# Optimization experiments

Hardware: AMD Instinct MI355X
Metric: run time of the kernel (lower is better)

Reference implementation:

```python
import jax, jax.numpy as jnp
import numpy as np

N = 100000
E = 3200000
IN_DIM = 128
HD = 64
HEADS = 4
NEG_SLOPE = 0.2


def setup_inputs() -> dict:
    key = jax.random.key(0)
    ks = jax.random.split(key, 12)
    s = lambda fan_in: 1.0 / np.sqrt(fan_in)
    x = jax.random.normal(ks[0], (N, IN_DIM), dtype=jnp.float32)
    edge_index = jax.random.randint(ks[1], (2, E), 0, N, dtype=jnp.int64)
    W1 = jax.random.normal(ks[2], (IN_DIM, HEADS * HD), dtype=jnp.float32) * s(IN_DIM)
    a_src1 = jax.random.normal(ks[3], (HEADS, HD), dtype=jnp.float32) * s(HD)
    a_dst1 = jax.random.normal(ks[4], (HEADS, HD), dtype=jnp.float32) * s(HD)
    b1 = jnp.zeros((HEADS * HD,), dtype=jnp.float32)
    W2 = jax.random.normal(ks[5], (HEADS * HD, HD), dtype=jnp.float32) * s(HEADS * HD)
    a_src2 = jax.random.normal(ks[6], (1, HD), dtype=jnp.float32) * s(HD)
    a_dst2 = jax.random.normal(ks[7], (1, HD), dtype=jnp.float32) * s(HD)
    b2 = jnp.zeros((HD,), dtype=jnp.float32)
    lin_w = jax.random.normal(ks[8], (HD, 2), dtype=jnp.float32) * s(HD)
    lin_b = jnp.zeros((2,), dtype=jnp.float32)
    return {"x": x, "edge_index": edge_index, "W1": W1, "a_src1": a_src1,
            "a_dst1": a_dst1, "b1": b1, "W2": W2, "a_src2": a_src2,
            "a_dst2": a_dst2, "b2": b2, "lin_w": lin_w, "lin_b": lin_b}


def gat_conv(x, src, dst, W, a_src, a_dst, bias, heads, out_dim, concat):
    n = x.shape[0]
    h = (x @ W).reshape(n, heads, out_dim)                 # [N,H,D]
    alpha_s = jnp.einsum('nhd,hd->nh', h, a_src)           # [N,H]
    alpha_d = jnp.einsum('nhd,hd->nh', h, a_dst)           # [N,H]
    e = alpha_s[src] + alpha_d[dst]                        # [Etot,H]
    e = jnp.where(e > 0, e, NEG_SLOPE * e)                 # leaky relu
    m = jax.ops.segment_max(e, dst, num_segments=n)        # scatter-softmax (stable)
    m = jnp.where(jnp.isfinite(m), m, 0.0)
    e = jnp.exp(e - m[dst])
    denom = jax.ops.segment_sum(e, dst, num_segments=n)
    alpha = e / denom[dst]                                 # [Etot,H]
    out = jax.ops.segment_sum(h[src] * alpha[:, :, None], dst, num_segments=n)  # [N,H,D]
    out = out.reshape(n, heads * out_dim) if concat else out.mean(axis=1)
    return out + bias


def reference(x, edge_index, W1, a_src1, a_dst1, b1, W2, a_src2, a_dst2, b2, lin_w, lin_b):
    n = x.shape[0]
    loops = jnp.arange(n, dtype=edge_index.dtype)
    src = jnp.concatenate([edge_index[0], loops])          # add self-loops (PyG default)
    dst = jnp.concatenate([edge_index[1], loops])
    h = gat_conv(x, src, dst, W1, a_src1, a_dst1, b1, HEADS, HD, True)
    h = jax.nn.elu(h)
    h = gat_conv(h, src, dst, W2, a_src2, a_dst2, b2, 1, HD, True)
    h = jax.nn.elu(h)
    return h @ lin_w + lin_b                               # [N,2]
```

## Files before the change

### kernel.cpp

```cpp
#include <hip/hip_runtime.h>
#include <hip/hip_fp16.h>
#include <math.h>

#define NN 100000
#define EE 3200000
#define ETOT (EE + NN)
#define NEG_SLOPE 0.2f
#define DMAX 96
#define CHUNK 4096
#define NB0 ((ETOT + CHUNK - 1) / CHUNK)
#define RB 391
#define CAP 16384

typedef _Float16 half8 __attribute__((ext_vector_type(8)));
typedef _Float16 half4v __attribute__((ext_vector_type(4)));
typedef float floatx4 __attribute__((ext_vector_type(4)));

__device__ __forceinline__ float wsum64(float v) {
#pragma unroll
  for (int o = 32; o; o >>= 1) v += __shfl_xor(v, o);
  return v;
}
__device__ __forceinline__ float lrelu(float v) { return v > 0.f ? v : NEG_SLOPE * v; }
__device__ __forceinline__ float elu1(float v) { return v > 0.f ? v : expm1f(v); }

__global__ void k_init(int* __restrict__ ccur) {
  ccur[threadIdx.x] = threadIdx.x * CAP;
}

__global__ __launch_bounds__(256) void k_pass1(const int* __restrict__ ei,
                                               int* __restrict__ ccur,
                                               unsigned* __restrict__ ebuf,
                                               const float* __restrict__ W1,
                                               const float* __restrict__ W2,
                                               _Float16* __restrict__ W1t,
                                               _Float16* __restrict__ W2t) {
  int b = blockIdx.x;
  if (b >= NB0) {
    int idx = (b - NB0) * 256 + threadIdx.x;
    if (idx < 32768) {
      int n = idx >> 7, k = idx & 127;
      W1t[idx] = (_Float16)W1[k * 256 + n];
    } else {
      int j = idx - 32768;
      int n = j >> 8, k = j & 255;
      W2t[j] = (_Float16)W2[k * 64 + n];
    }
    return;
  }
  __shared__ int h[256];
  __shared__ int cur[256];
  int t = threadIdx.x;
  h[t] = 0;
  __syncthreads();
  int base = b * CHUNK;
  int lim = base + CHUNK; if (lim > ETOT) lim = ETOT;
  for (int e = base + t; e < lim; e += 256) {
    int d = (e < EE) ? ei[EE + e] : (e - EE);
    atomicAdd(&h[(unsigned)d / (unsigned)RB], 1);
  }
  __syncthreads();
  if (h[t]) cur[t] = atomicAdd(&ccur[t], h[t]);
  __syncthreads();
  for (int e = base + t; e < lim; e += 256) {
    int s, d;
    if (e < EE) { s = ei[e]; d = ei[EE + e]; } else { s = e - EE; d = s; }
    unsigned cb = (unsigned)d / (unsigned)RB;
    unsigned dloc = (unsigned)d - cb * (unsigned)RB;
    int pos = atomicAdd(&cur[cb], 1);
    ebuf[pos] = (dloc << 17) | (unsigned)s;
  }
}

__global__ __launch_bounds__(256) void k_pass2(const unsigned* __restrict__ ebuf,
                                               const int* __restrict__ ccur,
                                               int* __restrict__ offs,
                                               int* __restrict__ degarr,
                                               int* __restrict__ csr) {
  __shared__ unsigned ed[CAP];
  __shared__ int hist[RB];
  __shared__ int cur[RB];
  int b = blockIdx.x, t = threadIdx.x;
  int d0 = b * RB;
  int rb = NN - d0; if (rb > RB) rb = RB;
  int w0 = b * CAP;
  int cnt = ccur[b] - w0;
  if (cnt > CAP) cnt = CAP;
  for (int j = t; j < rb; j += 256) hist[j] = 0;
  __syncthreads();
  for (int i = t; i < cnt; i += 256) {
    unsigned v = ebuf[w0 + i];
    ed[i] = v;
    atomicAdd(&hist[v >> 17], 1);
  }
  __syncthreads();
  if (t == 0) {
    int run = w0;
    for (int j = 0; j < rb; ++j) { cur[j] = run; run += hist[j]; }
  }
  __syncthreads();
  for (int j = t; j < rb; j += 256) {
    offs[d0 + j] = cur[j];
    degarr[d0 + j] = hist[j];
  }
  __syncthreads();
  for (int i = t; i < cnt; i += 256) {
    unsigned v = ed[i];
    int pos = atomicAdd(&cur[v >> 17], 1);
    csr[pos] = (int)(v & 0x1FFFFu);
  }
}

__global__ __launch_bounds__(256) void k_gemm1m(const float* __restrict__ x,
                                                const _Float16* __restrict__ W1t,
                                                const float* __restrict__ a_src,
                                                const float* __restrict__ a_dst,
                                                _Float16* __restrict__ h1h,
                                                float* __restrict__ as_out,
                                                float* __restrict__ ad_out) {
  __shared__ _Float16 As[64][136];
  __shared__ _Float16 Wt[128][136];
  const int bx = blockIdx.x & 1;
  const int by = blockIdx.x >> 1;
  const int tid = threadIdx.x;
  const int row0 = by * 64;
#pragma unroll
  for (int i = 0; i < 8; ++i) {
    int idx = i * 256 + tid;
    int r = idx >> 5;
    int c4 = (idx & 31) * 4;
    int gr = row0 + r;
    float4 f = make_float4(0.f, 0.f, 0.f, 0.f);
    if (gr < NN) f = *(const float4*)(x + (size_t)gr * 128 + c4);
    half4v h; h[0] = (_Float16)f.x; h[1] = (_Float16)f.y; h[2] = (_Float16)f.z; h[3] = (_Float16)f.w;
    *(half4v*)&As[r][c4] = h;
  }
#pragma unroll
  for (int i = 0; i < 8; ++i) {
    int idx = i * 256 + tid;
    int r = idx >> 4;
    int g = idx & 15;
    *(half8*)&Wt[r][g * 8] = *(const half8*)(W1t + (size_t)(bx * 128 + r) * 128 + g * 8);
  }
  __syncthreads();

  const int wid = tid >> 6, lane = tid & 63;
  const int m16 = lane & 15, quad = lane >> 4;
  floatx4 acc[8];
#pragma unroll
  for (int nt = 0; nt < 8; ++nt) acc[nt] = (floatx4){0.f, 0.f, 0.f, 0.f};
#pragma unroll
  for (int ks = 0; ks < 4; ++ks) {
    half8 av = *(half8*)&As[wid * 16 + m16][ks * 32 + quad * 8];
#pragma unroll
    for (int nt = 0; nt < 8; ++nt) {
      half8 bv = *(half8*)&Wt[nt * 16 + m16][ks * 32 + quad * 8];
      acc[nt] = __builtin_amdgcn_mfma_f32_16x16x32_f16(av, bv, acc[nt], 0, 0, 0);
    }
  }
  float asr[8], adr[8];
#pragma unroll
  for (int nt = 0; nt < 8; ++nt) {
    asr[nt] = a_src[bx * 128 + nt * 16 + m16];
    adr[nt] = a_dst[bx * 128 + nt * 16 + m16];
  }
#pragma unroll
  for (int r = 0; r < 4; ++r) {
    int gr = row0 + wid * 16 + quad * 4 + r;
    bool ok = gr < NN;
#pragma unroll
    for (int hp = 0; hp < 2; ++hp) {
      float ps = 0.f, pd = 0.f;
#pragma unroll
      for (int j = 0; j < 4; ++j) {
        ps = fmaf(acc[hp * 4 + j][r], asr[hp * 4 + j], ps);
        pd = fmaf(acc[hp * 4 + j][r], adr[hp * 4 + j], pd);
      }
#pragma unroll
      for (int o = 1; o < 16; o <<= 1) { ps += __shfl_xor(ps, o); pd += __shfl_xor(pd, o); }
      if (ok && m16 == 0) {
        as_out[gr * 4 + bx * 2 + hp] = ps;
        ad_out[gr * 4 + bx * 2 + hp] = pd;
      }
    }
    if (ok) {
#pragma unroll
      for (int nt = 0; nt < 8; ++nt)
        h1h[(size_t)gr * 256 + bx * 128 + nt * 16 + m16] = (_Float16)acc[nt][r];
    }
  }
}

__global__ __launch_bounds__(256) void k_gemm2m(const _Float16* __restrict__ h1e,
                                                const _Float16* __restrict__ W2t,
                                                const float* __restrict__ a_src,
                                                const float* __restrict__ a_dst,
                                                _Float16* __restrict__ h2h,
                                                float* __restrict__ as_out,
                                                float* __restrict__ ad_out) {
  __shared__ _Float16 As2[64][136];
  __shared__ _Float16 Wt2[64][264];
  const int by = blockIdx.x;
  const int tid = threadIdx.x;
  const int row0 = by * 64;
#pragma unroll
  for (int i = 0; i < 8; ++i) {
    int idx = i * 256 + tid;
    int r = idx >> 5;
    int g = idx & 31;
    *(half8*)&Wt2[r][g * 8] = *(const half8*)(W2t + (size_t)r * 256 + g * 8);
  }
  const int wid = tid >> 6, lane = tid & 63;
  const int m16 = lane & 15, quad = lane >> 4;
  floatx4 acc[4];
#pragma unroll
  for (int nt = 0; nt < 4; ++nt) acc[nt] = (floatx4){0.f, 0.f, 0.f, 0.f};

  for (int kc = 0; kc < 2; ++kc) {
#pragma unroll
    for (int i = 0; i < 4; ++i) {
      int idx = i * 256 + tid;
      int r = idx >> 4;
      int g = idx & 15;
      int gr = row0 + r;
      half8 v = {0, 0, 0, 0, 0, 0, 0, 0};
      if (gr < NN) v = *(const half8*)(h1e + (size_t)gr * 256 + kc * 128 + g * 8);
      *(half8*)&As2[r][g * 8] = v;
    }
    __syncthreads();
#pragma unroll
    for (int ks = 0; ks < 4; ++ks) {
      half8 av = *(half8*)&As2[wid * 16 + m16][ks * 32 + quad * 8];
#pragma unroll
      for (int nt = 0; nt < 4; ++nt) {
        half8 bv = *(half8*)&Wt2[nt * 16 + m16][kc * 128 + ks * 32 + quad * 8];
        acc[nt] = __builtin_amdgcn_mfma_f32_16x16x32_f16(av, bv, acc[nt], 0, 0, 0);
      }
    }
    __syncthreads();
  }
  float asr[4], adr[4];
#pragma unroll
  for (int nt = 0; nt < 4; ++nt) {
    asr[nt] = a_src[nt * 16 + m16];
    adr[nt] = a_dst[nt * 16 + m16];
  }
#pragma unroll
  for (int r = 0; r < 4; ++r) {
    float ps = 0.f, pd = 0.f;
#pragma unroll
    for (int nt = 0; nt < 4; ++nt) {
      ps = fmaf(acc[nt][r], asr[nt], ps);
      pd = fmaf(acc[nt][r], adr[nt], pd);
    }
#pragma unroll
    for (int o = 1; o < 16; o <<= 1) { ps += __shfl_xor(ps, o); pd += __shfl_xor(pd, o); }
    int gr = row0 + wid * 16 + quad * 4 + r;
    if (gr < NN) {
      if (m16 == 0) { as_out[gr] = ps; ad_out[gr] = pd; }
#pragma unroll
      for (int nt = 0; nt < 4; ++nt)
        h2h[(size_t)gr * 64 + nt * 16 + m16] = (_Float16)acc[nt][r];
    }
  }
}

__global__ __launch_bounds__(256) void k_attn1(const int* __restrict__ offs,
                                               const int* __restrict__ degarr,
                                               const int* __restrict__ csr_src,
                                               const float* __restrict__ a_s,
                                               const float* __restrict__ a_d,
                                               const _Float16* __restrict__ h1h,
                                               const float* __restrict__ b1,
                                               _Float16* __restrict__ h1e) {
  __shared__ float alpha[4][DMAX][4];
  __shared__ int sidx[4][DMAX];
  const int wid = threadIdx.x >> 6;
  const int n = blockIdx.x * 4 + wid;
  const int lane = threadIdx.x & 63;
  const int beg = offs[n], deg = degarr[n];
  const float4 ad = *(const float4*)(a_d + n * 4);
  float4 sm = make_float4(0.f, 0.f, 0.f, 0.f);
  for (int d = lane; d < deg; d += 64) {
    int s = csr_src[beg + d];
    float4 as = *(const float4*)(a_s + s * 4);
    float e0 = __expf(lrelu(as.x + ad.x));
    float e1 = __expf(lrelu(as.y + ad.y));
    float e2 = __expf(lrelu(as.z + ad.z));
    float e3 = __expf(lrelu(as.w + ad.w));
    sm.x += e0; sm.y += e1; sm.z += e2; sm.w += e3;
    if (d < DMAX) {
      sidx[wid][d] = s;
      *(float4*)&alpha[wid][d][0] = make_float4(e0, e1, e2, e3);
    }
  }
  sm.x = wsum64(sm.x); sm.y = wsum64(sm.y); sm.z = wsum64(sm.z); sm.w = wsum64(sm.w);
  const float4 inv4 = make_float4(1.f / sm.x, 1.f / sm.y, 1.f / sm.z, 1.f / sm.w);
  const int dlim = deg < DMAX ? deg : DMAX;
  for (int d = lane; d < dlim; d += 64) {
    float4 a = *(float4*)&alpha[wid][d][0];
    a.x *= inv4.x; a.y *= inv4.y; a.z *= inv4.z; a.w *= inv4.w;
    *(float4*)&alpha[wid][d][0] = a;
  }
  const int h = lane >> 4;
  float4 acc = make_float4(0.f, 0.f, 0.f, 0.f);
  int d = 0;
  for (; d + 8 <= dlim; d += 8) {
    int ss[8]; float ww[8];
#pragma unroll
    for (int u = 0; u < 8; ++u) {
      ss[u] = sidx[wid][d + u];
      ww[u] = alpha[wid][d + u][h];
    }
    half4v rr[8];
#pragma unroll
    for (int u = 0; u < 8; ++u)
      rr[u] = *(const half4v*)(h1h + (size_t)ss[u] * 256 + lane * 4);
#pragma unroll
    for (int u = 0; u < 8; ++u) {
      acc.x = fmaf((float)rr[u][0], ww[u], acc.x);
      acc.y = fmaf((float)rr[u][1], ww[u], acc.y);
      acc.z = fmaf((float)rr[u][2], ww[u], acc.z);
      acc.w = fmaf((float)rr[u][3], ww[u], acc.w);
    }
  }
  for (; d < dlim; ++d) {
    int s = sidx[wid][d];
    float w = alpha[wid][d][h];
    half4v r = *(const half4v*)(h1h + (size_t)s * 256 + lane * 4);
    acc.x = fmaf((float)r[0], w, acc.x); acc.y = fmaf((float)r[1], w, acc.y);
    acc.z = fmaf((float)r[2], w, acc.z); acc.w = fmaf((float)r[3], w, acc.w);
  }
  const float adh = (h & 2) ? ((h & 1) ? ad.w : ad.z) : ((h & 1) ? ad.y : ad.x);
  const float invh = (h & 2) ? ((h & 1) ? inv4.w : inv4.z) : ((h & 1) ? inv4.y : inv4.x);
  for (; d < deg; ++d) {
    int s = csr_src[beg + d];
    float w = __expf(lrelu(a_s[s * 4 + h] + adh)) * invh;
    half4v r = *(const half4v*)(h1h + (size_t)s * 256 + lane * 4);
    acc.x = fmaf((float)r[0], w, acc.x); acc.y = fmaf((float)r[1], w, acc.y);
    acc.z = fmaf((float)r[2], w, acc.z); acc.w = fmaf((float)r[3], w, acc.w);
  }
  const int c = lane * 4;
  float4 bb = *(const float4*)(b1 + c);
  half4v o;
  o[0] = (_Float16)elu1(acc.x + bb.x);
  o[1] = (_Float16)elu1(acc.y + bb.y);
  o[2] = (_Float16)elu1(acc.z + bb.z);
  o[3] = (_Float16)elu1(acc.w + bb.w);
  *(half4v*)(h1e + (size_t)n * 256 + c) = o;
}

__global__ __launch_bounds__(256) void k_attn2(const int* __restrict__ offs,
                                               const int* __restrict__ degarr,
                                               const int* __restrict__ csr_src,
                                               const float* __restrict__ a_s,
                                               const float* __restrict__ a_d,
                                               const _Float16* __restrict__ h2h,
                                               const float* __restrict__ b2,
                                               const float* __restrict__ lin_w,
                                               const float* __restrict__ lin_b,
                                               float* __restrict__ out) {
  __shared__ float alpha2[4][DMAX];
  __shared__ int sidx2[4][DMAX];
  const int wid = threadIdx.x >> 6;
  const int n = blockIdx.x * 4 + wid;
  const int lane = threadIdx.x & 63;
  const int beg = offs[n], deg = degarr[n];
  const float adn = a_d[n];
  float sm = 0.f;
  for (int d = lane; d < deg; d += 64) {
    int s = csr_src[beg + d];
    float e = __expf(lrelu(a_s[s] + adn));
    sm += e;
    if (d < DMAX) { sidx2[wid][d] = s; alpha2[wid][d] = e; }
  }
  sm = wsum64(sm);
  const float inv = 1.f / sm;
  const int dlim = deg < DMAX ? deg : DMAX;
  for (int d = lane; d < dlim; d += 64) alpha2[wid][d] *= inv;
  const int quarter = lane >> 4;
  const int fl = lane & 15;
  float acc4[4];
#pragma unroll
  for (int i = 0; i < 4; ++i) acc4[i] = 0.f;
  for (int d = 0; d < dlim; d += 8) {
    int ss[2]; float ww[2];
#pragma unroll
    for (int u = 0; u < 2; ++u) {
      int e = d + 4 * u + quarter;
      bool valid = e < dlim;
      int e2 = valid ? e : 0;
      ss[u] = sidx2[wid][e2];
      ww[u] = valid ? alpha2[wid][e2] : 0.f;
    }
    half4v rr[2];
#pragma unroll
    for (int u = 0; u < 2; ++u)
      rr[u] = *(const half4v*)(h2h + (size_t)ss[u] * 64 + fl * 4);
#pragma unroll
    for (int u = 0; u < 2; ++u)
#pragma unroll
      for (int i = 0; i < 4; ++i)
        acc4[i] = fmaf((float)rr[u][i], ww[u], acc4[i]);
  }
  for (int d = dlim + quarter; d < deg; d += 4) {
    int s = csr_src[beg + d];
    float w = __expf(lrelu(a_s[s] + adn)) * inv;
    half4v r = *(const half4v*)(h2h + (size_t)s * 64 + fl * 4);
#pragma unroll
    for (int i = 0; i < 4; ++i) acc4[i] = fmaf((float)r[i], w, acc4[i]);
  }
#pragma unroll
  for (int i = 0; i < 4; ++i) {
    acc4[i] += __shfl_xor(acc4[i], 16);
    acc4[i] += __shfl_xor(acc4[i], 32);
  }
  float p0 = 0.f, p1 = 0.f;
#pragma unroll
  for (int i = 0; i < 4; ++i) {
    float o = elu1(acc4[i] + b2[fl * 4 + i]);
    p0 = fmaf(o, lin_w[(fl * 4 + i) * 2 + 0], p0);
    p1 = fmaf(o, lin_w[(fl * 4 + i) * 2 + 1], p1);
  }
#pragma unroll
  for (int o = 1; o < 16; o <<= 1) { p0 += __shfl_xor(p0, o); p1 += __shfl_xor(p1, o); }
  if (lane == 0) {
    out[n * 2 + 0] = p0 + lin_b[0];
    out[n * 2 + 1] = p1 + lin_b[1];
  }
}

extern "C" void kernel_launch(void* const* d_in, const int* in_sizes, int n_in,
                              void* d_out, int out_size, void* d_ws, size_t ws_size,
                              hipStream_t stream) {
  const float* x      = (const float*)d_in[0];
  const int*   ei     = (const int*)d_in[1];
  const float* W1     = (const float*)d_in[2];
  const float* a_src1 = (const float*)d_in[3];
  const float* a_dst1 = (const float*)d_in[4];
  const float* b1     = (const float*)d_in[5];
  const float* W2     = (const float*)d_in[6];
  const float* a_src2 = (const float*)d_in[7];
  const float* a_dst2 = (const float*)d_in[8];
  const float* b2     = (const float*)d_in[9];
  const float* lin_w  = (const float*)d_in[10];
  const float* lin_b  = (const float*)d_in[11];
  float* outp = (float*)d_out;

  char* w = (char*)d_ws;
  _Float16* h1h = (_Float16*)(w + 0);
  _Float16* h1e = (_Float16*)(w + 51200000);
  _Float16* h2h = (_Float16*)(w + 102400000);
  _Float16* W1t = (_Float16*)(w + 115200000);
  _Float16* W2t = (_Float16*)(w + 115265536);
  float*  as1 = (float*)(w + 115298304);
  float*  ad1 = (float*)(w + 116898304);
  float*  as2 = (float*)(w + 118498304);
  float*  ad2 = (float*)(w + 118898304);
  int*    offs = (int*)(w + 119298304);
  int*    degarr = (int*)(w + 119698304);
  int*    ccur = (int*)(w + 120098304);
  unsigned* ebuf = (unsigned*)(w + 120099328);
  int*    csr = (int*)(w + 136876544);

  k_init<<<1, 256, 0, stream>>>(ccur);
  k_pass1<<<NB0 + 192, 256, 0, stream>>>(ei, ccur, ebuf, W1, W2, W1t, W2t);
  k_pass2<<<256, 256, 0, stream>>>(ebuf, ccur, offs, degarr, csr);

  k_gemm1m<<<2 * 1563, 256, 0, stream>>>(x, W1t, a_src1, a_dst1, h1h, as1, ad1);
  k_attn1<<<NN / 4, 256, 0, stream>>>(offs, degarr, csr, as1, ad1, h1h, b1, h1e);

  k_gemm2m<<<1563, 256, 0, stream>>>(h1e, W2t, a_src2, a_dst2, h2h, as2, ad2);
  k_attn2<<<NN / 4, 256, 0, stream>>>(offs, degarr, csr, as2, ad2, h2h, b2, lin_w, lin_b, outp);
}
```

Baseline: 615.5 us.

## Use sub-wavefront groups per node in attention kernels and memset counters

```diff
diff --git a/kernel.cpp b/kernel.cpp
--- a/kernel.cpp
+++ b/kernel.cpp
@@ -16,17 +16,8 @@
 typedef _Float16 half4v __attribute__((ext_vector_type(4)));
 typedef float floatx4 __attribute__((ext_vector_type(4)));
 
-__device__ __forceinline__ float wsum64(float v) {
-#pragma unroll
-  for (int o = 32; o; o >>= 1) v += __shfl_xor(v, o);
-  return v;
-}
 __device__ __forceinline__ float lrelu(float v) { return v > 0.f ? v : NEG_SLOPE * v; }
 __device__ __forceinline__ float elu1(float v) { return v > 0.f ? v : expm1f(v); }
-
-__global__ void k_init(int* __restrict__ ccur) {
-  ccur[threadIdx.x] = threadIdx.x * CAP;
-}
 
 __global__ __launch_bounds__(256) void k_pass1(const int* __restrict__ ei,
                                                int* __restrict__ ccur,
@@ -60,7 +51,7 @@
     atomicAdd(&h[(unsigned)d / (unsigned)RB], 1);
   }
   __syncthreads();
-  if (h[t]) cur[t] = atomicAdd(&ccur[t], h[t]);
+  if (h[t]) cur[t] = t * CAP + atomicAdd(&ccur[t], h[t]);
   __syncthreads();
   for (int e = base + t; e < lim; e += 256) {
     int s, d;
@@ -84,7 +75,7 @@
   int d0 = b * RB;
   int rb = NN - d0; if (rb > RB) rb = RB;
   int w0 = b * CAP;
-  int cnt = ccur[b] - w0;
+  int cnt = ccur[b];
   if (cnt > CAP) cnt = CAP;
   for (int j = t; j < rb; j += 256) hist[j] = 0;
   __syncthreads();
@@ -273,81 +264,90 @@
                                                const _Float16* __restrict__ h1h,
                                                const float* __restrict__ b1,
                                                _Float16* __restrict__ h1e) {
-  __shared__ float alpha[4][DMAX][4];
-  __shared__ int sidx[4][DMAX];
-  const int wid = threadIdx.x >> 6;
-  const int n = blockIdx.x * 4 + wid;
-  const int lane = threadIdx.x & 63;
+  __shared__ float alpha[8][DMAX][4];
+  __shared__ int sidx[8][DMAX];
+  const int g = threadIdx.x >> 5;
+  const int gl = threadIdx.x & 31;
+  const int n = blockIdx.x * 8 + g;
   const int beg = offs[n], deg = degarr[n];
-  const float4 ad = *(const float4*)(a_d + n * 4);
+  const float4 ad = *(const float4*)(a_d + (size_t)n * 4);
   float4 sm = make_float4(0.f, 0.f, 0.f, 0.f);
-  for (int d = lane; d < deg; d += 64) {
+  for (int d = gl; d < deg; d += 32) {
     int s = csr_src[beg + d];
-    float4 as = *(const float4*)(a_s + s * 4);
+    float4 as = *(const float4*)(a_s + (size_t)s * 4);
     float e0 = __expf(lrelu(as.x + ad.x));
     float e1 = __expf(lrelu(as.y + ad.y));
     float e2 = __expf(lrelu(as.z + ad.z));
     float e3 = __expf(lrelu(as.w + ad.w));
     sm.x += e0; sm.y += e1; sm.z += e2; sm.w += e3;
     if (d < DMAX) {
-      sidx[wid][d] = s;
-      *(float4*)&alpha[wid][d][0] = make_float4(e0, e1, e2, e3);
-    }
-  }
-  sm.x = wsum64(sm.x); sm.y = wsum64(sm.y); sm.z = wsum64(sm.z); sm.w = wsum64(sm.w);
+      sidx[g][d] = s;
+      *(float4*)&alpha[g][d][0] = make_float4(e0, e1, e2, e3);
+    }
+  }
+#pragma unroll
+  for (int o = 16; o; o >>= 1) {
+    sm.x += __shfl_xor(sm.x, o); sm.y += __shfl_xor(sm.y, o);
+    sm.z += __shfl_xor(sm.z, o); sm.w += __shfl_xor(sm.w, o);
+  }
   const float4 inv4 = make_float4(1.f / sm.x, 1.f / sm.y, 1.f / sm.z, 1.f / sm.w);
   const int dlim = deg < DMAX ? deg : DMAX;
-  for (int d = lane; d < dlim; d += 64) {
-    float4 a = *(float4*)&alpha[wid][d][0];
+  for (int d = gl; d < dlim; d += 32) {
+    float4 a = *(float4*)&alpha[g][d][0];
     a.x *= inv4.x; a.y *= inv4.y; a.z *= inv4.z; a.w *= inv4.w;
-    *(float4*)&alpha[wid][d][0] = a;
-  }
-  const int h = lane >> 4;
-  float4 acc = make_float4(0.f, 0.f, 0.f, 0.f);
+    *(float4*)&alpha[g][d][0] = a;
+  }
+  const int h = gl >> 3;
+  float acc8[8];
+#pragma unroll
+  for (int i = 0; i < 8; ++i) acc8[i] = 0.f;
   int d = 0;
   for (; d + 8 <= dlim; d += 8) {
     int ss[8]; float ww[8];
 #pragma unroll
     for (int u = 0; u < 8; ++u) {
-      ss[u] = sidx[wid][d + u];
-      ww[u] = alpha[wid][d + u][h];
-    }
-    half4v rr[8];
+      ss[u] = sidx[g][d + u];
+      ww[u] = alpha[g][d + u][h];
+    }
+    half8 rr[8];
 #pragma unroll
     for (int u = 0; u < 8; ++u)
-      rr[u] = *(const half4v*)(h1h + (size_t)ss[u] * 256 + lane * 4);
-#pragma unroll
-    for (int u = 0; u < 8; ++u) {
-      acc.x = fmaf((float)rr[u][0], ww[u], acc.x);
-      acc.y = fmaf((float)rr[u][1], ww[u], acc.y);
-      acc.z = fmaf((float)rr[u][2], ww[u], acc.z);
-      acc.w = fmaf((float)rr[u][3], ww[u], acc.w);
-    }
+      rr[u] = *(const half8*)(h1h + (size_t)ss[u] * 256 + gl * 8);
+#pragma unroll
+    for (int u = 0; u < 8; ++u)
+#pragma unroll
+      for (int i = 0; i < 8; ++i)
+        acc8[i] = fmaf((float)rr[u][i], ww[u], acc8[i]);
   }
   for (; d < dlim; ++d) {
-    int s = sidx[wid][d];
-    float w = alpha[wid][d][h];
-    half4v r = *(const half4v*)(h1h + (size_t)s * 256 + lane * 4);
-    acc.x = fmaf((float)r[0], w, acc.x); acc.y = fmaf((float)r[1], w, acc.y);
-    acc.z = fmaf((float)r[2], w, acc.z); acc.w = fmaf((float)r[3], w, acc.w);
+    int s = sidx[g][d];
+    float w = alpha[g][d][h];
+    half8 r = *(const half8*)(h1h + (size_t)s * 256 + gl * 8);
+#pragma unroll
+    for (int i = 0; i < 8; ++i) acc8[i] = fmaf((float)r[i], w, acc8[i]);
   }
   const float adh = (h & 2) ? ((h & 1) ? ad.w : ad.z) : ((h & 1) ? ad.y : ad.x);
   const float invh = (h & 2) ? ((h & 1) ? inv4.w : inv4.z) : ((h & 1) ? inv4.y : inv4.x);
   for (; d < deg; ++d) {
     int s = csr_src[beg + d];
-    float w = __expf(lrelu(a_s[s * 4 + h] + adh)) * invh;
-    half4v r = *(const half4v*)(h1h + (size_t)s * 256 + lane * 4);
-    acc.x = fmaf((float)r[0], w, acc.x); acc.y = fmaf((float)r[1], w, acc.y);
-    acc.z = fmaf((float)r[2], w, acc.z); acc.w = fmaf((float)r[3], w, acc.w);
-  }
-  const int c = lane * 4;
-  float4 bb = *(const float4*)(b1 + c);
-  half4v o;
-  o[0] = (_Float16)elu1(acc.x + bb.x);
-  o[1] = (_Float16)elu1(acc.y + bb.y);
-  o[2] = (_Float16)elu1(acc.z + bb.z);
-  o[3] = (_Float16)elu1(acc.w + bb.w);
-  *(half4v*)(h1e + (size_t)n * 256 + c) = o;
+    float w = __expf(lrelu(a_s[(size_t)s * 4 + h] + adh)) * invh;
+    half8 r = *(const half8*)(h1h + (size_t)s * 256 + gl * 8);
+#pragma unroll
+    for (int i = 0; i < 8; ++i) acc8[i] = fmaf((float)r[i], w, acc8[i]);
+  }
+  const int c = gl * 8;
+  float4 bb0 = *(const float4*)(b1 + c);
+  float4 bb1 = *(const float4*)(b1 + c + 4);
+  half8 o;
+  o[0] = (_Float16)elu1(acc8[0] + bb0.x);
+  o[1] = (_Float16)elu1(acc8[1] + bb0.y);
+  o[2] = (_Float16)elu1(acc8[2] + bb0.z);
+  o[3] = (_Float16)elu1(acc8[3] + bb0.w);
+  o[4] = (_Float16)elu1(acc8[4] + bb1.x);
+  o[5] = (_Float16)elu1(acc8[5] + bb1.y);
+  o[6] = (_Float16)elu1(acc8[6] + bb1.z);
+  o[7] = (_Float16)elu1(acc8[7] + bb1.w);
+  *(half8*)(h1e + (size_t)n * 256 + c) = o;
 }
 
 __global__ __launch_bounds__(256) void k_attn2(const int* __restrict__ offs,
@@ -360,71 +360,70 @@
                                                const float* __restrict__ lin_w,
                                                const float* __restrict__ lin_b,
                                                float* __restrict__ out) {
-  __shared__ float alpha2[4][DMAX];
-  __shared__ int sidx2[4][DMAX];
-  const int wid = threadIdx.x >> 6;
-  const int n = blockIdx.x * 4 + wid;
-  const int lane = threadIdx.x & 63;
+  __shared__ float alpha2[16][DMAX];
+  __shared__ int sidx2[16][DMAX];
+  const int g = threadIdx.x >> 4;
+  const int gl = threadIdx.x & 15;
+  const int n = blockIdx.x * 16 + g;
   const int beg = offs[n], deg = degarr[n];
   const float adn = a_d[n];
   float sm = 0.f;
-  for (int d = lane; d < deg; d += 64) {
+  for (int d = gl; d < deg; d += 16) {
     int s = csr_src[beg + d];
     float e = __expf(lrelu(a_s[s] + adn));
     sm += e;
-    if (d < DMAX) { sidx2[wid][d] = s; alpha2[wid][d] = e; }
-  }
-  sm = wsum64(sm);
+    if (d < DMAX) { sidx2[g][d] = s; alpha2[g][d] = e; }
+  }
+#pragma unroll
+  for (int o = 8; o; o >>= 1) sm += __shfl_xor(sm, o);
   const float inv = 1.f / sm;
   const int dlim = deg < DMAX ? deg : DMAX;
-  for (int d = lane; d < dlim; d += 64) alpha2[wid][d] *= inv;
-  const int quarter = lane >> 4;
-  const int fl = lane & 15;
+  for (int d = gl; d < dlim; d += 16) alpha2[g][d] *= inv;
   float acc4[4];
 #pragma unroll
   for (int i = 0; i < 4; ++i) acc4[i] = 0.f;
-  for (int d = 0; d < dlim; d += 8) {
-    int ss[2]; float ww[2];
-#pragma unroll
-    for (int u = 0; u < 2; ++u) {
-      int e = d + 4 * u + quarter;
-      bool valid = e < dlim;
-      int e2 = valid ? e : 0;
-      ss[u] = sidx2[wid][e2];
-      ww[u] = valid ? alpha2[wid][e2] : 0.f;
-    }
-    half4v rr[2];
-#pragma unroll
-    for (int u = 0; u < 2; ++u)
-      rr[u] = *(const half4v*)(h2h + (size_t)ss[u] * 64 + fl * 4);
-#pragma unroll
-    for (int u = 0; u < 2; ++u)
+  int d = 0;
+  for (; d + 8 <= dlim; d += 8) {
+    int ss[8]; float ww[8];
+#pragma unroll
+    for (int u = 0; u < 8; ++u) {
+      ss[u] = sidx2[g][d + u];
+      ww[u] = alpha2[g][d + u];
+    }
+    half4v rr[8];
+#pragma unroll
+    for (int u = 0; u < 8; ++u)
+      rr[u] = *(const half4v*)(h2h + (size_t)ss[u] * 64 + gl * 4);
+#pragma unroll
+    for (int u = 0; u < 8; ++u)
 #pragma unroll
       for (int i = 0; i < 4; ++i)
         acc4[i] = fmaf((float)rr[u][i], ww[u], acc4[i]);
   }
-  for (int d = dlim + quarter; d < deg; d += 4) {
+  for (; d < dlim; ++d) {
+    int s = sidx2[g][d];
+    float w = alpha2[g][d];
+    half4v r = *(const half4v*)(h2h + (size_t)s * 64 + gl * 4);
+#pragma unroll
+    for (int i = 0; i < 4; ++i) acc4[i] = fmaf((float)r[i], w, acc4[i]);
+  }
+  for (; d < deg; ++d) {
     int s = csr_src[beg + d];
     float w = __expf(lrelu(a_s[s] + adn)) * inv;
-    half4v r = *(const half4v*)(h2h + (size_t)s * 64 + fl * 4);
+    half4v r = *(const half4v*)(h2h + (size_t)s * 64 + gl * 4);
 #pragma unroll
     for (int i = 0; i < 4; ++i) acc4[i] = fmaf((float)r[i], w, acc4[i]);
   }
+  float p0 = 0.f, p1 = 0.f;
 #pragma unroll
   for (int i = 0; i < 4; ++i) {
-    acc4[i] += __shfl_xor(acc4[i], 16);
-    acc4[i] += __shfl_xor(acc4[i], 32);
-  }
-  float p0 = 0.f, p1 = 0.f;
-#pragma unroll
-  for (int i = 0; i < 4; ++i) {
-    float o = elu1(acc4[i] + b2[fl * 4 + i]);
-    p0 = fmaf(o, lin_w[(fl * 4 + i) * 2 + 0], p0);
-    p1 = fmaf(o, lin_w[(fl * 4 + i) * 2 + 1], p1);
-  }
-#pragma unroll
-  for (int o = 1; o < 16; o <<= 1) { p0 += __shfl_xor(p0, o); p1 += __shfl_xor(p1, o); }
-  if (lane == 0) {
+    float o = elu1(acc4[i] + b2[gl * 4 + i]);
+    p0 = fmaf(o, lin_w[(gl * 4 + i) * 2 + 0], p0);
+    p1 = fmaf(o, lin_w[(gl * 4 + i) * 2 + 1], p1);
+  }
+#pragma unroll
+  for (int o = 8; o; o >>= 1) { p0 += __shfl_xor(p0, o); p1 += __shfl_xor(p1, o); }
+  if (gl == 0) {
     out[n * 2 + 0] = p0 + lin_b[0];
     out[n * 2 + 1] = p1 + lin_b[1];
   }
@@ -463,13 +462,13 @@
   unsigned* ebuf = (unsigned*)(w + 120099328);
   int*    csr = (int*)(w + 136876544);
 
-  k_init<<<1, 256, 0, stream>>>(ccur);
+  hipMemsetAsync(ccur, 0, 1024, stream);
   k_pass1<<<NB0 + 192, 256, 0, stream>>>(ei, ccur, ebuf, W1, W2, W1t, W2t);
   k_pass2<<<256, 256, 0, stream>>>(ebuf, ccur, offs, degarr, csr);
 
   k_gemm1m<<<2 * 1563, 256, 0, stream>>>(x, W1t, a_src1, a_dst1, h1h, as1, ad1);
-  k_attn1<<<NN / 4, 256, 0, stream>>>(offs, degarr, csr, as1, ad1, h1h, b1, h1e);
+  k_attn1<<<NN / 8, 256, 0, stream>>>(offs, degarr, csr, as1, ad1, h1h, b1, h1e);
 
   k_gemm2m<<<1563, 256, 0, stream>>>(h1e, W2t, a_src2, a_dst2, h2h, as2, ad2);
-  k_attn2<<<NN / 4, 256, 0, stream>>>(offs, degarr, csr, as2, ad2, h2h, b2, lin_w, lin_b, outp);
-}
+  k_attn2<<<NN / 16, 256, 0, stream>>>(offs, degarr, csr, as2, ad2, h2h, b2, lin_w, lin_b, outp);
+}
```

Measured after the change: 589.1 us. -4.3%, faster.
